# Kernel optimization log

Measured on AMD Instinct MI355X. Metric: run time of the kernel, lower is better.

Reference implementation:

```python
import jax, jax.numpy as jnp
import numpy as np

K = 8192            # codebook_size
DECAY = 0.99        # ema_decay
COMMIT = 0.25       # commitment_cost
ENT_RATIO = 0.1     # entropy_loss_ratio
ENT_TEMP = 1.0      # entropy_temperature
EPS = 1e-5


def setup_inputs() -> dict:
    key = jax.random.key(0)
    k1, k2, k3, k4 = jax.random.split(key, 4)
    x = jax.random.normal(k1, (32768, 256), dtype=jnp.float32)
    codebook = jax.random.normal(k2, (8192, 256), dtype=jnp.float32)
    cluster_size_ema = jax.random.uniform(k3, (8192,), dtype=jnp.float32)
    codebook_ema = jax.random.normal(k4, (8192, 256), dtype=jnp.float32)
    return {"x": x, "codebook": codebook,
            "cluster_size_ema": cluster_size_ema, "codebook_ema": codebook_ema}


def _entropy_loss(affinity, temperature):
    # affinity: [N, K]
    a = affinity / temperature
    probs = jax.nn.softmax(a, axis=-1)
    log_probs = jax.nn.log_softmax(a + 1e-5, axis=-1)
    avg_probs = jnp.mean(probs, axis=0)                      # [K]
    avg_entropy = -jnp.sum(avg_probs * jnp.log(avg_probs + 1e-5))
    sample_entropy = -jnp.mean(jnp.sum(probs * log_probs, axis=-1))
    return sample_entropy - avg_entropy


def reference(x, codebook, cluster_size_ema, codebook_ema):
    N, d = x.shape
    x2 = jnp.sum(x * x, axis=1, keepdims=True)               # [N,1]
    c2 = jnp.sum(codebook * codebook, axis=1)                # [K]
    d2 = x2 - 2.0 * (x @ codebook.T) + c2[None, :]           # [N,K]
    distances = jnp.sqrt(jnp.maximum(d2, 0.0))
    encoding_indices = jnp.argmin(distances, axis=1)         # [N]
    quantized = codebook[encoding_indices]                   # [N,d]

    # training losses (straight-through for output)
    e_latent_loss = jnp.mean((jax.lax.stop_gradient(quantized) - x) ** 2) * COMMIT
    q_latent_loss = jnp.mean((quantized - jax.lax.stop_gradient(x)) ** 2)
    ent = _entropy_loss(-distances, ENT_TEMP) * ENT_RATIO
    loss = e_latent_loss + q_latent_loss + ent

    # EMA codebook update (encodings.sum(0) and encodings^T @ x via segment sums)
    counts = jax.ops.segment_sum(jnp.ones((N,), x.dtype), encoding_indices,
                                 num_segments=K)             # [K]
    dw = jax.ops.segment_sum(x, encoding_indices, num_segments=K)  # [K,d]
    new_cluster_size_ema = DECAY * cluster_size_ema + (1.0 - DECAY) * counts
    new_codebook_ema = DECAY * codebook_ema + (1.0 - DECAY) * dw
    n = jnp.sum(new_cluster_size_ema)
    smoothed = (new_cluster_size_ema + EPS) / (n + K * EPS) * n
    new_codebook = new_codebook_ema / smoothed[:, None]

    quantized_st = x + jax.lax.stop_gradient(quantized - x)

    avg_probs = counts / N
    perplexity = jnp.exp(-jnp.sum(avg_probs * jnp.log(avg_probs + 1e-10)))

    return (quantized_st, loss, perplexity, encoding_indices,
            new_codebook, new_cluster_size_ema, new_codebook_ema)
```

## Files before the change

### kernel.cpp

```cpp
#include <hip/hip_runtime.h>
#include <math.h>

#define N_ROWS 32768
#define DIM 256
#define KCODES 8192

#define BM 128
#define BN 128
#define NSLICE 8
#define SLICE_K 1024
#define NKT (SLICE_K / BN)
#define NDT 4
#define NSTEP (NKT * NDT)
#define TAU 3e-3f

#define FAST_SQRT(x) __builtin_amdgcn_sqrtf(x)

#define WS_C2    0
#define WS_X2    8192
#define WS_BD    40960
#define WS_BI    73728
#define WS_L     106496
#define WS_FLAGL 139264
#define WS_AVGP  172032
#define WS_CNT   180224
#define WS_SCAL  188416
#define WS_FLAGN 188424

#define PF (NSLICE * N_ROWS)

typedef _Float16 f16x8 __attribute__((ext_vector_type(8)));
typedef float f32x4 __attribute__((ext_vector_type(4)));

__device__ __forceinline__ void gll16(const void* g, void* l) {
    __builtin_amdgcn_global_load_lds((const __attribute__((address_space(1))) void*)g,
                                     (__attribute__((address_space(3))) void*)l, 16, 0, 0);
}

__global__ void split_k(const float* __restrict__ src, ushort* __restrict__ h,
                        float* __restrict__ norms) {
    int tid = threadIdx.x;
    int i = blockIdx.x * 256 + tid;
    const float4* s4 = (const float4*)src;
    float4 v0 = s4[2 * i], v1 = s4[2 * i + 1];
    float vv[8] = {v0.x, v0.y, v0.z, v0.w, v1.x, v1.y, v1.z, v1.w};
    float nrm = 0.f;
    uint w[4];
    #pragma unroll
    for (int p = 0; p < 4; ++p) {
        float a = vv[2*p], b = vv[2*p+1];
        nrm = fmaf(a, a, nrm); nrm = fmaf(b, b, nrm);
        _Float16 ha = (_Float16)a, hb = (_Float16)b;
        w[p] = (uint)__builtin_bit_cast(unsigned short, ha)
             | ((uint)__builtin_bit_cast(unsigned short, hb) << 16);
    }
    ((uint4*)h)[i] = make_uint4(w[0], w[1], w[2], w[3]);
    #pragma unroll
    for (int off = 16; off >= 1; off >>= 1) nrm += __shfl_xor(nrm, off);
    if ((tid & 31) == 0) norms[blockIdx.x * 8 + (tid >> 5)] = nrm;
}

__global__ void init_ncbe_k(const float* __restrict__ cbe, float* __restrict__ outNcbe) {
    int i = blockIdx.x * 256 + threadIdx.x;
    float4 v = ((const float4*)cbe)[i];
    v.x *= 0.99f; v.y *= 0.99f; v.z *= 0.99f; v.w *= 0.99f;
    ((float4*)outNcbe)[i] = v;
}

__device__ __forceinline__ void online_merge(float& b1, int& i1, float& b2, float& l, float& T,
                                             float nb1, int ni1, float nb2, float nl, float nT) {
    float m  = fminf(b1, nb1);
    float fa = __expf(m - b1);
    float fb = __expf(m - nb1);
    float L  = fa * l + fb * nl;
    float TT = fa * (T + (m - b1) * l) + fb * (nT + (m - nb1) * nl);
    float losing = fmaxf(b1, nb1);
    float B2 = fminf(fminf(b2, nb2), losing);
    if (nb1 < b1 || (nb1 == b1 && ni1 < i1)) i1 = ni1;
    b1 = m; b2 = B2; l = L; T = TT;
}

template<int PASS>
__global__ __launch_bounds__(512, 4) void vq_mfma(const ushort* __restrict__ xf,
                                                  const ushort* __restrict__ cf,
                                                  float* __restrict__ ws,
                                                  float* __restrict__ P) {
    __shared__ __align__(16) char lds[2][32768];
    __shared__ __align__(16) float c2s[SLICE_K];
    __shared__ float sred[1536];

    const int tid  = threadIdx.x;
    const int lane = tid & 63, wid = tid >> 6;
    const int wcode = wid & 1, wx = wid >> 1;
    const int l15 = lane & 15, l4 = lane >> 4;
    const int slice = blockIdx.x & 7, chunk = blockIdx.x >> 3;
    const int rowBase = chunk * BM;

    c2s[tid]       = ws[WS_C2 + slice * SLICE_K + tid];
    c2s[tid + 512] = ws[WS_C2 + slice * SLICE_K + tid + 512];
    if (PASS == 2) { sred[tid] = 0.f; sred[tid + 512] = 0.f; }

    const char* cbB[2]; const char* xB[2]; int dCB[2], dX[2];
    #pragma unroll
    for (int j = 0; j < 2; ++j) {
        int q = j * 512 + tid;
        int row = q >> 3, c = tid & 7;
        int sw = (c ^ (row & 7)) << 4;
        cbB[j] = (const char*)cf + (((size_t)(slice * SLICE_K + row)) << 9) + sw;
        xB[j]  = (const char*)xf + (((size_t)(rowBase + row)) << 9) + sw;
        dCB[j] = q << 4;
        dX[j]  = 16384 + (q << 4);
    }

    float x2v[2], bdv[2], invl[2];
    #pragma unroll
    for (int n = 0; n < 2; ++n) {
        int rl = wx * 32 + n * 16 + l15;
        x2v[n] = ws[WS_X2 + rowBase + rl];
        if (PASS == 2) {
            bdv[n]  = ws[WS_BD + rowBase + rl];
            invl[n] = 1.0f / ws[WS_L + rowBase + rl];
        }
    }
    float rb1[2], rb2[2], rlv[2], rTv[2]; int ri1[2];
    #pragma unroll
    for (int n = 0; n < 2; ++n) { rb1[n] = 1e30f; rb2[n] = 1e30f; rlv[n] = 0.f; rTv[n] = 0.f; ri1[n] = 0; }

    #pragma unroll
    for (int j = 0; j < 2; ++j) {
        gll16(cbB[j], &lds[0][dCB[j]]);
        gll16(xB[j],  &lds[0][dX[j]]);
    }

    const int swkey = l15 & 7;

    for (int kt = 0; kt < NKT; ++kt) {
        f32x4 acc[4][2];
        #pragma unroll
        for (int m = 0; m < 4; ++m) {
            acc[m][0] = (f32x4){0.f, 0.f, 0.f, 0.f};
            acc[m][1] = (f32x4){0.f, 0.f, 0.f, 0.f};
        }

        #pragma unroll
        for (int dt = 0; dt < NDT; ++dt) {
            const int t = kt * 4 + dt;
            if (t + 1 < NSTEP) {
                const int t1 = t + 1;
                const int cbo = ((t1 >> 2) << 16) | ((t1 & 3) << 7);
                const int xo  = (t1 & 3) << 7;
                char* wb = &lds[t1 & 1][0];
                #pragma unroll
                for (int j = 0; j < 2; ++j) {
                    gll16(cbB[j] + cbo, wb + dCB[j]);
                    gll16(xB[j] + xo,   wb + dX[j]);
                }
                asm volatile("s_waitcnt vmcnt(4)" ::: "memory");
            } else {
                asm volatile("s_waitcnt vmcnt(0)" ::: "memory");
            }
            __builtin_amdgcn_s_barrier();
            __builtin_amdgcn_sched_barrier(0);

            const char* bb = &lds[t & 1][0];
            #pragma unroll
            for (int s = 0; s < 2; ++s) {
                const int csw = (((s << 2) | l4) ^ swkey) << 4;
                f16x8 Bf[2];
                #pragma unroll
                for (int n = 0; n < 2; ++n)
                    Bf[n] = __builtin_bit_cast(f16x8,
                        *(const uint4*)(bb + 16384 + (wx * 32 + n * 16 + l15) * 128 + csw));
                __builtin_amdgcn_s_setprio(1);
                #pragma unroll
                for (int m = 0; m < 4; ++m) {
                    f16x8 Af = __builtin_bit_cast(f16x8,
                        *(const uint4*)(bb + (wcode * 64 + m * 16 + l15) * 128 + csw));
                    acc[m][0] = __builtin_amdgcn_mfma_f32_16x16x32_f16(Af, Bf[0], acc[m][0], 0, 0, 0);
                    acc[m][1] = __builtin_amdgcn_mfma_f32_16x16x32_f16(Af, Bf[1], acc[m][1], 0, 0, 0);
                }
                __builtin_amdgcn_s_setprio(0);
            }
            __builtin_amdgcn_sched_barrier(0);
            __builtin_amdgcn_s_barrier();
        }

        const int lcb = kt * BN + wcode * 64 + l4 * 4;
        if (PASS == 1) {
            #pragma unroll
            for (int n = 0; n < 2; ++n) {
                uint pm = ~0u, p2 = ~0u;
                float dsv[16];
                #pragma unroll
                for (int m = 0; m < 4; ++m) {
                    float4 c2v = *(const float4*)&c2s[lcb + m * 16];
                    #pragma unroll
                    for (int r = 0; r < 4; ++r) {
                        float d2 = fmaf(-2.f, acc[m][n][r], x2v[n] + ((const float*)&c2v)[r]);
                        float dv = FAST_SQRT(fmaxf(d2, 0.f));
                        dsv[m * 4 + r] = dv;
                        uint pk = (__float_as_uint(dv) & 0xFFFFFFF0u) | (uint)(m * 4 + r);
                        bool lt = pk < pm;
                        uint alt = (pk < p2) ? pk : p2;
                        p2 = lt ? pm : alt;
                        pm = lt ? pk : pm;
                    }
                }
                uint cand = pm & 15u;
                float b1  = __uint_as_float(pm & 0xFFFFFFF0u);
                float b2v = __uint_as_float(p2 & 0xFFFFFFF0u);
                int   i1  = slice * SLICE_K + lcb + (int)((cand >> 2) << 4) + (int)(cand & 3u);
                float ls = 0.f, ts = 0.f;
                #pragma unroll
                for (int q = 0; q < 16; ++q) {
                    float u = b1 - dsv[q];
                    float e = __expf(u);
                    ls += e;
                    ts = fmaf(e, u, ts);
                }
                online_merge(rb1[n], ri1[n], rb2[n], rlv[n], rTv[n], b1, i1, b2v, ls, ts);
            }
        } else {
            float ps[4][4];
            #pragma unroll
            for (int m = 0; m < 4; ++m)
                #pragma unroll
                for (int r = 0; r < 4; ++r) ps[m][r] = 0.f;
            #pragma unroll
            for (int n = 0; n < 2; ++n) {
                #pragma unroll
                for (int m = 0; m < 4; ++m) {
                    float4 c2v = *(const float4*)&c2s[lcb + m * 16];
                    #pragma unroll
                    for (int r = 0; r < 4; ++r) {
                        float d2 = fmaf(-2.f, acc[m][n][r], x2v[n] + ((const float*)&c2v)[r]);
                        float dv = FAST_SQRT(fmaxf(d2, 0.f));
                        ps[m][r] = fmaf(__expf(bdv[n] - dv), invl[n], ps[m][r]);
                    }
                }
            }
            #pragma unroll
            for (int m = 0; m < 4; ++m)
                #pragma unroll
                for (int r = 0; r < 4; ++r) {
                    float v = ps[m][r];
                    v += __shfl_xor(v, 1); v += __shfl_xor(v, 2);
                    v += __shfl_xor(v, 4); v += __shfl_xor(v, 8);
                    ps[m][r] = v;
                }
            if (l15 == 0) {
                #pragma unroll
                for (int m = 0; m < 4; ++m)
                    #pragma unroll
                    for (int r = 0; r < 4; ++r)
                        atomicAdd(&sred[lcb + m * 16 + r], ps[m][r]);
            }
        }
    }

    if (PASS == 1) {
        #pragma unroll
        for (int n = 0; n < 2; ++n) {
            #pragma unroll
            for (int off = 16; off <= 32; off <<= 1) {
                float ob1 = __shfl_xor(rb1[n], off);
                int   oi  = __shfl_xor(ri1[n], off);
                float ob2 = __shfl_xor(rb2[n], off);
                float ol  = __shfl_xor(rlv[n], off);
                float oT  = __shfl_xor(rTv[n], off);
                online_merge(rb1[n], ri1[n], rb2[n], rlv[n], rTv[n], ob1, oi, ob2, ol, oT);
            }
        }
        if (l4 == 0) {
            #pragma unroll
            for (int n = 0; n < 2; ++n) {
                int rl = wx * 32 + n * 16 + l15;
                sred[(rl << 1) + wcode]       = rb1[n];
                sred[256 + (rl << 1) + wcode] = rb2[n];
                sred[512 + (rl << 1) + wcode] = rlv[n];
                sred[768 + (rl << 1) + wcode] = rTv[n];
                ((int*)sred)[1024 + (rl << 1) + wcode] = ri1[n];
            }
        }
        __syncthreads();
        if (tid < BM) {
            float b1 = sred[tid * 2];       int i1 = ((int*)sred)[1024 + tid * 2];
            float b2 = sred[256 + tid * 2];
            float L  = sred[512 + tid * 2];
            float T  = sred[768 + tid * 2];
            online_merge(b1, i1, b2, L, T,
                         sred[tid * 2 + 1], ((int*)sred)[1024 + tid * 2 + 1],
                         sred[256 + tid * 2 + 1], sred[512 + tid * 2 + 1], sred[768 + tid * 2 + 1]);
            int grow = rowBase + tid;
            P[0 * PF + slice * N_ROWS + grow] = b1;
            P[1 * PF + slice * N_ROWS + grow] = b2;
            P[2 * PF + slice * N_ROWS + grow] = L;
            P[3 * PF + slice * N_ROWS + grow] = T;
            ((int*)P)[4 * PF + slice * N_ROWS + grow] = i1;
        }
    } else {
        __syncthreads();
        atomicAdd(&ws[WS_AVGP + slice * SLICE_K + tid], sred[tid]);
        atomicAdd(&ws[WS_AVGP + slice * SLICE_K + tid + 512], sred[tid + 512]);
    }
}

__global__ void merge_k(const float* __restrict__ P, float* __restrict__ ws,
                        unsigned long long* __restrict__ enc) {
    const int tid = threadIdx.x, lane = tid & 63;
    const int row = blockIdx.x * 256 + tid;
    float b1 = 1e30f, b2 = 1e30f, L = 0.f, T = 0.f; int i1 = 0;
    #pragma unroll
    for (int s = 0; s < NSLICE; ++s) {
        float nb1 = P[0 * PF + s * N_ROWS + row];
        float nb2 = P[1 * PF + s * N_ROWS + row];
        float nl  = P[2 * PF + s * N_ROWS + row];
        float nT  = P[3 * PF + s * N_ROWS + row];
        int   ni  = ((const int*)P)[4 * PF + s * N_ROWS + row];
        online_merge(b1, i1, b2, L, T, nb1, ni, nb2, nl, nT);
    }
    ws[WS_BD + row] = b1;
    ((int*)ws)[WS_BI + row] = i1;
    ws[WS_L + row] = L;
    if (b2 - b1 < TAU) {
        int p = atomicAdd(((int*)ws) + WS_FLAGN, 1);
        ((int*)ws)[WS_FLAGL + p] = row;
        enc[p] = ~0ULL;
    }
    float sval = T / L - __logf(L);
    #pragma unroll
    for (int off = 32; off >= 1; off >>= 1) sval += __shfl_xor(sval, off);
    if (lane == 0) atomicAdd(&ws[WS_SCAL + 1], sval);
}

__global__ __launch_bounds__(256) void fixup_k(const float* __restrict__ x,
                                               const float* __restrict__ cb,
                                               float* __restrict__ ws,
                                               unsigned long long* __restrict__ enc) {
    __shared__ __align__(16) float xrow[DIM];
    const int tid = threadIdx.x, lane = tid & 63, wid = tid >> 6;
    const int slice = blockIdx.x & 7;
    const int nf = ((const int*)ws)[WS_FLAGN];
    const int c0 = slice * SLICE_K + wid * 256;
    for (int fi = blockIdx.x >> 3; fi < nf; fi += (gridDim.x >> 3)) {
        const int row = ((const int*)ws)[WS_FLAGL + fi];
        __syncthreads();
        if (tid < 64) ((float4*)xrow)[tid] = ((const float4*)(x + (size_t)row * DIM))[tid];
        __syncthreads();
        const float x2r = ws[WS_X2 + row];
        const float4 xv = ((const float4*)xrow)[lane];
        unsigned long long best = ~0ULL;
        for (int j = 0; j < 256; ++j) {
            const int c = c0 + j;
            float4 cv = ((const float4*)(cb + (size_t)c * DIM))[lane];
            float dot = cv.x * xv.x;
            dot = fmaf(cv.y, xv.y, dot);
            dot = fmaf(cv.z, xv.z, dot);
            dot = fmaf(cv.w, xv.w, dot);
            #pragma unroll
            for (int off = 1; off <= 32; off <<= 1) dot += __shfl_xor(dot, off);
            float d2 = fmaxf(fmaf(-2.f, dot, x2r + ws[WS_C2 + c]), 0.f);
            float dv = sqrtf(d2);
            unsigned long long e = (((unsigned long long)__float_as_uint(dv)) << 32)
                                 | (unsigned int)c;
            best = (e < best) ? e : best;
        }
        if (lane == 0) atomicMin(&enc[fi], best);
    }
}

__global__ void unpack_k(const unsigned long long* __restrict__ enc, float* __restrict__ ws) {
    int f = blockIdx.x * 256 + threadIdx.x;
    int nf = ((const int*)ws)[WS_FLAGN];
    if (f < nf) {
        int row = ((const int*)ws)[WS_FLAGL + f];
        ((int*)ws)[WS_BI + row] = (int)(enc[f] & 0xFFFFFFFFu);
    }
}

__global__ void gather_k(const float* __restrict__ x, const float* __restrict__ cb,
                         float* __restrict__ ws, float* __restrict__ outQ,
                         float* __restrict__ outNcbe, float* __restrict__ outIdxF) {
    __shared__ float red2[4];
    const int tid = threadIdx.x, w = tid >> 6, lane = tid & 63;
    float msum = 0.f;
    for (int it = 0; it < 8; ++it) {
        int n = blockIdx.x * 32 + it * 4 + w;
        int idx = ((const int*)ws)[WS_BI + n];
        float4 xv = ((const float4*)(x + (size_t)n * DIM))[lane];
        float4 cv = ((const float4*)(cb + (size_t)idx * DIM))[lane];
        ((float4*)(outQ + (size_t)n * DIM))[lane] = cv;
        float* dst = outNcbe + (size_t)idx * DIM + lane * 4;
        const float g = 0.01f;
        atomicAdd(dst + 0, g * xv.x); atomicAdd(dst + 1, g * xv.y);
        atomicAdd(dst + 2, g * xv.z); atomicAdd(dst + 3, g * xv.w);
        float dx = cv.x - xv.x, dy = cv.y - xv.y, dz = cv.z - xv.z, dw = cv.w - xv.w;
        float s = dx*dx + dy*dy + dz*dz + dw*dw;
        #pragma unroll
        for (int off = 32; off >= 1; off >>= 1) s += __shfl_xor(s, off);
        if (lane == 0) {
            msum += s;
            atomicAdd(&ws[WS_CNT + idx], 1.0f);
            outIdxF[n] = (float)idx;
        }
    }
    if (lane == 0) red2[w] = msum;
    __syncthreads();
    if (tid == 0) atomicAdd(&ws[WS_SCAL + 0], red2[0] + red2[1] + red2[2] + red2[3]);
}

__global__ void stats_k(const float* __restrict__ cse, float* __restrict__ ws,
                        float* __restrict__ outNcse) {
    int tid = threadIdx.x, lane = tid & 63;
    int k = blockIdx.x * 256 + tid;
    float cnt = ws[WS_CNT + k];
    float ncse = 0.99f * cse[k] + 0.01f * cnt;
    outNcse[k] = ncse;
    float ap  = ws[WS_AVGP + k] * (1.0f / N_ROWS);
    float ae  = -(ap * __logf(ap + 1e-5f));
    float app = cnt * (1.0f / N_ROWS);
    float pe  = -(app * __logf(app + 1e-10f));
    #pragma unroll
    for (int off = 32; off >= 1; off >>= 1) {
        ncse += __shfl_xor(ncse, off);
        ae   += __shfl_xor(ae, off);
        pe   += __shfl_xor(pe, off);
    }
    if (lane == 0) {
        atomicAdd(&ws[WS_SCAL + 4], ncse);
        atomicAdd(&ws[WS_SCAL + 2], ae);
        atomicAdd(&ws[WS_SCAL + 3], pe);
    }
}

__global__ void newcb_k(const float* __restrict__ ws, const float* __restrict__ outNcse,
                        const float* __restrict__ outNcbe, float* __restrict__ outNc) {
    int w = threadIdx.x >> 6, lane = threadIdx.x & 63;
    int k = blockIdx.x * 4 + w;
    float n = ws[WS_SCAL + 4];
    float ncse = outNcse[k];
    float smoothed = (ncse + 1e-5f) / (n + (float)KCODES * 1e-5f) * n;
    float inv = 1.0f / smoothed;
    float4 v = ((const float4*)(outNcbe + (size_t)k * DIM))[lane];
    v.x *= inv; v.y *= inv; v.z *= inv; v.w *= inv;
    ((float4*)(outNc + (size_t)k * DIM))[lane] = v;
}

__global__ void finalize_k(const float* __restrict__ ws, float* __restrict__ outLoss,
                           float* __restrict__ outPerp) {
    float mse  = ws[WS_SCAL + 0] * (1.0f / ((float)N_ROWS * 256.0f));
    float sent = -ws[WS_SCAL + 1] * (1.0f / (float)N_ROWS);
    float ent  = sent - ws[WS_SCAL + 2];
    outLoss[0] = 1.25f * mse + 0.1f * ent;
    outPerp[0] = expf(ws[WS_SCAL + 3]);
}

extern "C" void kernel_launch(void* const* d_in, const int* in_sizes, int n_in,
                              void* d_out, int out_size, void* d_ws, size_t ws_size,
                              hipStream_t stream) {
    const float* x   = (const float*)d_in[0];
    const float* cb  = (const float*)d_in[1];
    const float* cse = (const float*)d_in[2];
    const float* cbe = (const float*)d_in[3];
    float* out = (float*)d_out;
    float* ws  = (float*)d_ws;

    float* outQ    = out;
    float* outLoss = out + 8388608;
    float* outPerp = out + 8388609;
    float* outIdxF = out + 8388610;
    float* outNc   = out + 8421378;
    float* outNcse = out + 10518530;
    float* outNcbe = out + 10526722;

    ushort* xf = (ushort*)outQ;
    ushort* cf = (ushort*)(out + 8421380);
    float*  P  = outNcbe;
    unsigned long long* enc = (unsigned long long*)(outNcbe + 5 * PF);

    (void)hipMemsetAsync(ws + WS_AVGP, 0, (size_t)(WS_FLAGN + 1 - WS_AVGP) * sizeof(float), stream);
    split_k<<<N_ROWS * DIM / 2048, 256, 0, stream>>>(x, xf, ws + WS_X2);
    split_k<<<KCODES * DIM / 2048, 256, 0, stream>>>(cb, cf, ws + WS_C2);
    vq_mfma<1><<<NSLICE * (N_ROWS / BM), 512, 0, stream>>>(xf, cf, ws, P);
    merge_k<<<N_ROWS / 256, 256, 0, stream>>>(P, ws, enc);
    vq_mfma<2><<<NSLICE * (N_ROWS / BM), 512, 0, stream>>>(xf, cf, ws, P);
    fixup_k<<<2048, 256, 0, stream>>>(x, cb, ws, enc);
    unpack_k<<<N_ROWS / 256, 256, 0, stream>>>(enc, ws);
    init_ncbe_k<<<2048, 256, 0, stream>>>(cbe, outNcbe);
    gather_k<<<1024, 256, 0, stream>>>(x, cb, ws, outQ, outNcbe, outIdxF);
    stats_k<<<KCODES / 256, 256, 0, stream>>>(cse, ws, outNcse);
    newcb_k<<<KCODES / 4, 256, 0, stream>>>(ws, outNcse, outNcbe, outNc);
    finalize_k<<<1, 1, 0, stream>>>(ws, outLoss, outPerp);
}
```

Measured before the change: 1.021 ms.

## Prune fixup rescoring to candidate slices and restructure per-row dot product

The merge step now records, for each ambiguous row, a bitmask of the slices whose local best distance lies within a small epsilon of the global best, and lowers the ambiguity threshold. The fixup kernel skips slices outside that mask. It also has each wave score four codes at a time using 16-lane groups holding x in registers, and caches the slice's squared norms in LDS. This cuts the exact fp32 recheck work and shuffle count, at the risk of missing the true argmin if the half-precision distance error exceeds the new thresholds.

```diff
diff --git a/kernel.cpp b/kernel.cpp
--- a/kernel.cpp
+++ b/kernel.cpp
@@ -12,7 +12,8 @@
 #define NKT (SLICE_K / BN)
 #define NDT 4
 #define NSTEP (NKT * NDT)
-#define TAU 3e-3f
+#define TAU 2e-3f
+#define EPS2 4e-3f
 
 #define FAST_SQRT(x) __builtin_amdgcn_sqrtf(x)
 
@@ -310,6 +311,7 @@
     const int tid = threadIdx.x, lane = tid & 63;
     const int row = blockIdx.x * 256 + tid;
     float b1 = 1e30f, b2 = 1e30f, L = 0.f, T = 0.f; int i1 = 0;
+    float sb1[NSLICE];
     #pragma unroll
     for (int s = 0; s < NSLICE; ++s) {
         float nb1 = P[0 * PF + s * N_ROWS + row];
@@ -317,14 +319,19 @@
         float nl  = P[2 * PF + s * N_ROWS + row];
         float nT  = P[3 * PF + s * N_ROWS + row];
         int   ni  = ((const int*)P)[4 * PF + s * N_ROWS + row];
+        sb1[s] = nb1;
         online_merge(b1, i1, b2, L, T, nb1, ni, nb2, nl, nT);
     }
     ws[WS_BD + row] = b1;
     ((int*)ws)[WS_BI + row] = i1;
     ws[WS_L + row] = L;
     if (b2 - b1 < TAU) {
+        uint mask = 0;
+        #pragma unroll
+        for (int s = 0; s < NSLICE; ++s)
+            if (sb1[s] <= b1 + EPS2) mask |= (1u << s);
         int p = atomicAdd(((int*)ws) + WS_FLAGN, 1);
-        ((int*)ws)[WS_FLAGL + p] = row;
+        ((uint*)ws)[WS_FLAGL + p] = (uint)row | (mask << 20);
         enc[p] = ~0ULL;
     }
     float sval = T / L - __logf(L);
@@ -337,34 +344,49 @@
                                                const float* __restrict__ cb,
                                                float* __restrict__ ws,
                                                unsigned long long* __restrict__ enc) {
-    __shared__ __align__(16) float xrow[DIM];
+    __shared__ __align__(16) float c2sl[SLICE_K];
     const int tid = threadIdx.x, lane = tid & 63, wid = tid >> 6;
+    const int g = lane >> 4, l15 = lane & 15;
     const int slice = blockIdx.x & 7;
+    for (int i = tid; i < SLICE_K; i += 256) c2sl[i] = ws[WS_C2 + slice * SLICE_K + i];
+    __syncthreads();
     const int nf = ((const int*)ws)[WS_FLAGN];
-    const int c0 = slice * SLICE_K + wid * 256;
+    const int cbase = slice * SLICE_K + wid * 256;
     for (int fi = blockIdx.x >> 3; fi < nf; fi += (gridDim.x >> 3)) {
-        const int row = ((const int*)ws)[WS_FLAGL + fi];
-        __syncthreads();
-        if (tid < 64) ((float4*)xrow)[tid] = ((const float4*)(x + (size_t)row * DIM))[tid];
-        __syncthreads();
+        const uint entry = ((const uint*)ws)[WS_FLAGL + fi];
+        if (!((entry >> 20) & (1u << slice))) continue;
+        const int row = (int)(entry & 0xFFFFFu);
+        const float4* xp = (const float4*)(x + (size_t)row * DIM) + l15 * 4;
+        float4 xr0 = xp[0], xr1 = xp[1], xr2 = xp[2], xr3 = xp[3];
         const float x2r = ws[WS_X2 + row];
-        const float4 xv = ((const float4*)xrow)[lane];
         unsigned long long best = ~0ULL;
-        for (int j = 0; j < 256; ++j) {
-            const int c = c0 + j;
-            float4 cv = ((const float4*)(cb + (size_t)c * DIM))[lane];
-            float dot = cv.x * xv.x;
-            dot = fmaf(cv.y, xv.y, dot);
-            dot = fmaf(cv.z, xv.z, dot);
-            dot = fmaf(cv.w, xv.w, dot);
-            #pragma unroll
-            for (int off = 1; off <= 32; off <<= 1) dot += __shfl_xor(dot, off);
-            float d2 = fmaxf(fmaf(-2.f, dot, x2r + ws[WS_C2 + c]), 0.f);
+        #pragma unroll 4
+        for (int j = 0; j < 64; ++j) {
+            const int c = cbase + j * 4 + g;
+            const float4* cp = (const float4*)(cb + (size_t)c * DIM) + l15 * 4;
+            float4 c0 = cp[0], c1 = cp[1], c2 = cp[2], c3 = cp[3];
+            float dot = c0.x * xr0.x;
+            dot = fmaf(c0.y, xr0.y, dot); dot = fmaf(c0.z, xr0.z, dot); dot = fmaf(c0.w, xr0.w, dot);
+            dot = fmaf(c1.x, xr1.x, dot); dot = fmaf(c1.y, xr1.y, dot);
+            dot = fmaf(c1.z, xr1.z, dot); dot = fmaf(c1.w, xr1.w, dot);
+            dot = fmaf(c2.x, xr2.x, dot); dot = fmaf(c2.y, xr2.y, dot);
+            dot = fmaf(c2.z, xr2.z, dot); dot = fmaf(c2.w, xr2.w, dot);
+            dot = fmaf(c3.x, xr3.x, dot); dot = fmaf(c3.y, xr3.y, dot);
+            dot = fmaf(c3.z, xr3.z, dot); dot = fmaf(c3.w, xr3.w, dot);
+            dot += __shfl_xor(dot, 1); dot += __shfl_xor(dot, 2);
+            dot += __shfl_xor(dot, 4); dot += __shfl_xor(dot, 8);
+            float d2 = fmaxf(fmaf(-2.f, dot, x2r + c2sl[wid * 256 + j * 4 + g]), 0.f);
             float dv = sqrtf(d2);
             unsigned long long e = (((unsigned long long)__float_as_uint(dv)) << 32)
                                  | (unsigned int)c;
             best = (e < best) ? e : best;
         }
+        {
+            unsigned long long o = __shfl_xor(best, 16);
+            best = (o < best) ? o : best;
+            o = __shfl_xor(best, 32);
+            best = (o < best) ? o : best;
+        }
         if (lane == 0) atomicMin(&enc[fi], best);
     }
 }
@@ -373,7 +395,7 @@
     int f = blockIdx.x * 256 + threadIdx.x;
     int nf = ((const int*)ws)[WS_FLAGN];
     if (f < nf) {
-        int row = ((const int*)ws)[WS_FLAGL + f];
+        int row = (int)(((const uint*)ws)[WS_FLAGL + f] & 0xFFFFFu);
         ((int*)ws)[WS_BI + row] = (int)(enc[f] & 0xFFFFFFFFu);
     }
 }
```

Measured after the change: 871.6 us. 1.17x faster.
